# Kernel tuning notes

Hardware: AMD Instinct MI355X
Metric: run time of the kernel (lower is better)

## Reference

```python
import jax, jax.numpy as jnp
import numpy as np

IN_F, OUT_F = 4096, 11008
TOKENS = 8

def setup_inputs() -> dict:
    key = jax.random.key(0)
    k1, k2, k3, k4, k5, k6 = jax.random.split(key, 6)
    x = jax.random.normal(k1, (TOKENS, IN_F), dtype=jnp.float32)
    base_weight = jax.random.normal(k2, (OUT_F, IN_F), dtype=jnp.float32) * 0.02
    q_delta = jax.random.randint(k3, (OUT_F, IN_F), 0, 16, dtype=jnp.int32)
    scales = jax.random.uniform(k4, (OUT_F,), dtype=jnp.float32) * 1e-3 + 1e-8
    zero_points = jax.random.normal(k5, (OUT_F,), dtype=jnp.float32)
    bias = jax.random.normal(k6, (OUT_F,), dtype=jnp.float32) * 0.01
    return {"x": x, "base_weight": base_weight, "q_delta": q_delta,
            "scales": scales, "zero_points": zero_points, "bias": bias}

def reference(x, base_weight, q_delta, scales, zero_points, bias):
    # per-channel dequantize: delta[o,i] = (q[o,i] - zp[o]) * scale[o]
    delta = (q_delta.astype(jnp.float32) - zero_points[:, None]) * scales[:, None]
    w = base_weight + delta  # [out, in]
    return jnp.dot(x, w.T) + bias  # [tokens, out]
```

## Files before the change

### kernel.cpp

```cpp
#include <hip/hip_runtime.h>


#define IN_F    4096
#define OUT_F   11008
#define TOKENS  8
#define RPB     8
#define THREADS 256
#define NBLOCKS (OUT_F / RPB)

typedef float vf4 __attribute__((ext_vector_type(4)));
typedef int   vi4 __attribute__((ext_vector_type(4)));

__global__ __launch_bounds__(THREADS, 2)
void DeltaQuantLinear_87540023427416_kernel(
    const float* __restrict__ x,
    const float* __restrict__ w,
    const int*   __restrict__ q,
    const float* __restrict__ scales,
    const float* __restrict__ zps,
    const float* __restrict__ bias,
    float*       __restrict__ out)
{
    __shared__ float lds[32 * 257];
    __shared__ float lds2[32 * 8];

    const int tid = threadIdx.x;
    const int o0  = blockIdx.x * RPB;

    float s[RPB], c0[RPB];
#pragma unroll
    for (int r = 0; r < RPB; ++r) {
        const float sc = scales[o0 + r];
        s[r]  = sc;
        c0[r] = -zps[o0 + r] * sc;
    }

    float acc[RPB][TOKENS];
#pragma unroll
    for (int r = 0; r < RPB; ++r)
#pragma unroll
        for (int t = 0; t < TOKENS; ++t) acc[r][t] = 0.0f;

#pragma unroll 1
    for (int c = 0; c < 4; ++c) {
        const int kbase = c * 1024 + tid * 4;

        vf4 xr[TOKENS];
#pragma unroll
        for (int t = 0; t < TOKENS; ++t)
            xr[t] = *(const vf4*)(x + t * IN_F + kbase);

#pragma unroll
        for (int g = 0; g < 2; ++g) {
            vf4 wv[4];
            vi4 qv[4];
#pragma unroll
            for (int rr = 0; rr < 4; ++rr) {
                const int r = g * 4 + rr;
                const float* wp = w + (size_t)(o0 + r) * IN_F + kbase;
                const int*   qp = q + (size_t)(o0 + r) * IN_F + kbase;
                wv[rr] = __builtin_nontemporal_load((const vf4*)wp);
                qv[rr] = __builtin_nontemporal_load((const vi4*)qp);
            }
#pragma unroll
            for (int rr = 0; rr < 4; ++rr) {
                const int r = g * 4 + rr;
#pragma unroll
                for (int j = 0; j < 4; ++j) {
                    const float wfull = fmaf((float)qv[rr][j], s[r], wv[rr][j] + c0[r]);
#pragma unroll
                    for (int t = 0; t < TOKENS; ++t) {
                        acc[r][t] = fmaf(xr[t][j], wfull, acc[r][t]);
                    }
                }
            }
        }
    }

#pragma unroll
    for (int h = 0; h < 2; ++h) {
#pragma unroll
        for (int rl = 0; rl < 4; ++rl)
#pragma unroll
            for (int t = 0; t < TOKENS; ++t)
                lds[(rl * 8 + t) * 257 + tid] = acc[h * 4 + rl][t];
        __syncthreads();

        {
            const int l = tid & 31;
            const int p = tid >> 5;
            float sum = 0.0f;
            const float* row = &lds[l * 257 + p * 32];
#pragma unroll
            for (int j = 0; j < 32; ++j) sum += row[j];
            lds2[l * 8 + p] = sum;
        }
        __syncthreads();

        if (tid < 32) {
            float tot = 0.0f;
#pragma unroll
            for (int j = 0; j < 8; ++j) tot += lds2[tid * 8 + j];
            const int rl = tid >> 3;
            const int t  = tid & 7;
            const int o  = o0 + h * 4 + rl;
            out[t * OUT_F + o] = tot + bias[o];
        }
        __syncthreads();
    }
}

extern "C" void kernel_launch(void* const* d_in, const int* in_sizes, int n_in,
                              void* d_out, int out_size, void* d_ws, size_t ws_size,
                              hipStream_t stream) {
    const float* x      = (const float*)d_in[0];
    const float* w      = (const float*)d_in[1];
    const int*   q      = (const int*)d_in[2];
    const float* scales = (const float*)d_in[3];
    const float* zps    = (const float*)d_in[4];
    const float* bias   = (const float*)d_in[5];
    float* out = (float*)d_out;

    DeltaQuantLinear_87540023427416_kernel<<<NBLOCKS, THREADS, 0, stream>>>(
        x, w, q, scales, zps, bias, out);
}
```

Measured before the change: 350.0 us.

## Halve rows per block and double-buffer weight/q loads across K chunks

Each block now handles 4 output rows instead of 8, which doubles the grid to 2752 blocks. Weight and quantized-delta vector loads for the next K chunk are issued before computing on the current chunk, using a two-stage register buffer. The reduction becomes a single pass. The aim is more memory-level parallelism for this bandwidth-bound GEMV. In exchange, x is re-read by twice as many blocks, and the double-buffered registers raise register pressure.

```diff
diff --git a/kernel.cpp b/kernel.cpp
--- a/kernel.cpp
+++ b/kernel.cpp
@@ -4,7 +4,7 @@
 #define IN_F    4096
 #define OUT_F   11008
 #define TOKENS  8
-#define RPB     8
+#define RPB     4
 #define THREADS 256
 #define NBLOCKS (OUT_F / RPB)
 
@@ -41,72 +41,76 @@
 #pragma unroll
         for (int t = 0; t < TOKENS; ++t) acc[r][t] = 0.0f;
 
-#pragma unroll 1
+    const float* wbase = w + (size_t)o0 * IN_F + tid * 4;
+    const int*   qbase = q + (size_t)o0 * IN_F + tid * 4;
+
+    vf4 wv[2][RPB];
+    vi4 qv[2][RPB];
+
+#pragma unroll
+    for (int r = 0; r < RPB; ++r) {
+        wv[0][r] = __builtin_nontemporal_load((const vf4*)(wbase + (size_t)r * IN_F));
+        qv[0][r] = __builtin_nontemporal_load((const vi4*)(qbase + (size_t)r * IN_F));
+    }
+
+#pragma unroll
     for (int c = 0; c < 4; ++c) {
+        const int cur = c & 1;
+        const int nxt = cur ^ 1;
+
+        if (c < 3) {
+            const int koff = (c + 1) * 1024;
+#pragma unroll
+            for (int r = 0; r < RPB; ++r) {
+                wv[nxt][r] = __builtin_nontemporal_load((const vf4*)(wbase + (size_t)r * IN_F + koff));
+                qv[nxt][r] = __builtin_nontemporal_load((const vi4*)(qbase + (size_t)r * IN_F + koff));
+            }
+        }
+
         const int kbase = c * 1024 + tid * 4;
-
         vf4 xr[TOKENS];
 #pragma unroll
         for (int t = 0; t < TOKENS; ++t)
             xr[t] = *(const vf4*)(x + t * IN_F + kbase);
 
 #pragma unroll
-        for (int g = 0; g < 2; ++g) {
-            vf4 wv[4];
-            vi4 qv[4];
+        for (int r = 0; r < RPB; ++r) {
 #pragma unroll
-            for (int rr = 0; rr < 4; ++rr) {
-                const int r = g * 4 + rr;
-                const float* wp = w + (size_t)(o0 + r) * IN_F + kbase;
-                const int*   qp = q + (size_t)(o0 + r) * IN_F + kbase;
-                wv[rr] = __builtin_nontemporal_load((const vf4*)wp);
-                qv[rr] = __builtin_nontemporal_load((const vi4*)qp);
-            }
+            for (int j = 0; j < 4; ++j) {
+                const float wfull = fmaf((float)qv[cur][r][j], s[r], wv[cur][r][j] + c0[r]);
 #pragma unroll
-            for (int rr = 0; rr < 4; ++rr) {
-                const int r = g * 4 + rr;
-#pragma unroll
-                for (int j = 0; j < 4; ++j) {
-                    const float wfull = fmaf((float)qv[rr][j], s[r], wv[rr][j] + c0[r]);
-#pragma unroll
-                    for (int t = 0; t < TOKENS; ++t) {
-                        acc[r][t] = fmaf(xr[t][j], wfull, acc[r][t]);
-                    }
-                }
+                for (int t = 0; t < TOKENS; ++t)
+                    acc[r][t] = fmaf(xr[t][j], wfull, acc[r][t]);
             }
         }
     }
 
 #pragma unroll
-    for (int h = 0; h < 2; ++h) {
+    for (int r = 0; r < RPB; ++r)
 #pragma unroll
-        for (int rl = 0; rl < 4; ++rl)
+        for (int t = 0; t < TOKENS; ++t)
+            lds[(r * 8 + t) * 257 + tid] = acc[r][t];
+    __syncthreads();
+
+    {
+        const int l = tid & 31;
+        const int p = tid >> 5;
+        float sum = 0.0f;
+        const float* row = &lds[l * 257 + p * 32];
 #pragma unroll
-            for (int t = 0; t < TOKENS; ++t)
-                lds[(rl * 8 + t) * 257 + tid] = acc[h * 4 + rl][t];
-        __syncthreads();
+        for (int j = 0; j < 32; ++j) sum += row[j];
+        lds2[l * 8 + p] = sum;
+    }
+    __syncthreads();
 
-        {
-            const int l = tid & 31;
-            const int p = tid >> 5;
-            float sum = 0.0f;
-            const float* row = &lds[l * 257 + p * 32];
+    if (tid < 32) {
+        float tot = 0.0f;
 #pragma unroll
-            for (int j = 0; j < 32; ++j) sum += row[j];
-            lds2[l * 8 + p] = sum;
-        }
-        __syncthreads();
-
-        if (tid < 32) {
-            float tot = 0.0f;
-#pragma unroll
-            for (int j = 0; j < 8; ++j) tot += lds2[tid * 8 + j];
-            const int rl = tid >> 3;
-            const int t  = tid & 7;
-            const int o  = o0 + h * 4 + rl;
-            out[t * OUT_F + o] = tot + bias[o];
-        }
-        __syncthreads();
+        for (int j = 0; j < 8; ++j) tot += lds2[tid * 8 + j];
+        const int r = tid >> 3;
+        const int t = tid & 7;
+        const int o = o0 + r;
+        out[t * OUT_F + o] = tot + bias[o];
     }
 }
 
```

New measurement: 339.0 us. 3.1% less time.
